# Kernel tuning notes

Measured on AMD Instinct MI355X. Metric: run time of the kernel, lower is better.

The kernel has to match this reference:

```python
import jax, jax.numpy as jnp
import numpy as np

N_GROUPS = 32
N_HEADS = 8
GN_EPS = 1e-5


def setup_inputs() -> dict:
    key = jax.random.key(0)
    k1, k2, k3 = jax.random.split(key, 3)
    B, C, H, W = 8, 512, 32, 32
    x = jax.random.normal(k1, (B, C, H, W), dtype=jnp.float32)
    gn_w = jnp.ones((C,), dtype=jnp.float32)
    gn_b = jnp.zeros((C,), dtype=jnp.float32)
    qkv_w = jax.random.normal(k2, (3 * C, C), dtype=jnp.float32) * 0.02
    qkv_b = jnp.zeros((3 * C,), dtype=jnp.float32)
    proj_w = jax.random.normal(k3, (C, C), dtype=jnp.float32) * 0.02
    proj_b = jnp.zeros((C,), dtype=jnp.float32)
    return {"x": x, "gn_w": gn_w, "gn_b": gn_b, "qkv_w": qkv_w,
            "qkv_b": qkv_b, "proj_w": proj_w, "proj_b": proj_b}


def reference(x, gn_w, gn_b, qkv_w, qkv_b, proj_w, proj_b):
    b, c, h, w = x.shape
    t = h * w
    xf = x.reshape(b, c, t)

    # GroupNorm(32, C) over (channel-group, spatial) dims
    xg = xf.reshape(b, N_GROUPS, (c // N_GROUPS) * t)
    mean = jnp.mean(xg, axis=-1, keepdims=True)
    var = jnp.var(xg, axis=-1, keepdims=True)
    normed = ((xg - mean) * jax.lax.rsqrt(var + GN_EPS)).reshape(b, c, t)
    normed = normed * gn_w[None, :, None] + gn_b[None, :, None]

    # 1x1 Conv1d -> matmul over channel dim
    qkv = jnp.einsum('oc,bct->bot', qkv_w, normed) + qkv_b[None, :, None]
    q, k, v = jnp.split(qkv, 3, axis=1)  # each [b, c, t]

    ch = c // N_HEADS
    scale = 1.0 / np.sqrt(np.sqrt(ch)).astype(np.float32)
    q = (q * scale).reshape(b * N_HEADS, ch, t)
    k = (k * scale).reshape(b * N_HEADS, ch, t)
    v = v.reshape(b * N_HEADS, ch, t)

    weight = jnp.einsum('bct,bcs->bts', q, k)
    weight = jax.nn.softmax(weight.astype(jnp.float32), axis=-1).astype(q.dtype)
    a = jnp.einsum('bts,bcs->bct', weight, v).reshape(b, c, t)

    # residual + 1x1 Conv2d projection
    out = jnp.einsum('oc,bct->bot', proj_w, xf + a) + proj_b[None, :, None]
    return out.reshape(b, -1, h, w)
```

## Files before the change

kernel.cpp:

```cpp
#include <hip/hip_runtime.h>

constexpr int B = 8;
constexpr int C = 512;
constexpr int T = 1024;
constexpr int CPG = 16;
constexpr int NH = 8;
constexpr int CH = 64;
constexpr float GN_EPS = 1e-5f;
constexpr float QSCALE = 0.18033688011112042f;

typedef __attribute__((ext_vector_type(4))) float f32x4;
typedef __attribute__((ext_vector_type(8))) short bf16x8;
typedef __attribute__((ext_vector_type(4))) short bf16x4;

__device__ inline short f2bf(float f) {
  union { float f; unsigned u; } v; v.f = f;
  unsigned r = (v.u + 0x7FFFu + ((v.u >> 16) & 1u)) >> 16;
  return (short)r;
}

__device__ inline unsigned cvt_pk_bf16(float a, float b) {
  unsigned r;
  asm("v_cvt_pk_bf16_f32 %0, %1, %2" : "=v"(r) : "v"(a), "v"(b));
  return r;
}

#define GLOAD16(gsrc, ldst) __builtin_amdgcn_global_load_lds( \
    (const __attribute__((address_space(1))) unsigned int*)(gsrc), \
    (__attribute__((address_space(3))) unsigned int*)(ldst), 16, 0, 0)

__global__ __launch_bounds__(256)
void gnw_kernel(const float* __restrict__ x, const float* __restrict__ gw,
                const float* __restrict__ gb, short* __restrict__ out,
                const float* __restrict__ qw, const float* __restrict__ pw,
                short* __restrict__ qwb, short* __restrict__ pwb) {
  const int bid = blockIdx.x;
  if (bid >= 256) {
    const int idx = (bid - 256) * 256 + threadIdx.x;
    constexpr int QW4 = 3 * C * C / 4;
    float4 v;
    short* dst;
    if (idx < QW4) {
      v = ((const float4*)qw)[idx];
      dst = qwb + (size_t)idx * 4;
    } else {
      v = ((const float4*)pw)[idx - QW4];
      dst = pwb + (size_t)(idx - QW4) * 4;
    }
    bf16x4 o;
    o[0] = f2bf(v.x); o[1] = f2bf(v.y); o[2] = f2bf(v.z); o[3] = f2bf(v.w);
    *(bf16x4*)dst = o;
    return;
  }
  const int b = bid >> 5;
  const int g = bid & 31;
  const float* xp = x + (size_t)(b * C + g * CPG) * T;
  const float4* x4 = (const float4*)xp;
  float s = 0.f, ss = 0.f;
  for (int i = threadIdx.x; i < CPG * T / 4; i += 256) {
    float4 v = x4[i];
    s  += v.x + v.y + v.z + v.w;
    ss += v.x * v.x + v.y * v.y + v.z * v.z + v.w * v.w;
  }
  #pragma unroll
  for (int o = 32; o; o >>= 1) {
    s  += __shfl_down(s, o);
    ss += __shfl_down(ss, o);
  }
  __shared__ float rs[4], rss[4];
  __shared__ float sm, sr;
  const int wid = threadIdx.x >> 6;
  if ((threadIdx.x & 63) == 0) { rs[wid] = s; rss[wid] = ss; }
  __syncthreads();
  if (threadIdx.x == 0) {
    float ts  = rs[0] + rs[1] + rs[2] + rs[3];
    float tss = rss[0] + rss[1] + rss[2] + rss[3];
    constexpr float inv_n = 1.f / (CPG * T);
    float mean = ts * inv_n;
    float var = tss * inv_n - mean * mean;
    sm = mean;
    sr = rsqrtf(var + GN_EPS);
  }
  __syncthreads();
  const float mean = sm, rstd = sr;

  const int tid = threadIdx.x;
  const int cl = tid >> 4;
  const int t4 = (tid & 15) * 4;
  const float cw = gw[g * CPG + cl] * rstd;
  const float cb = gb[g * CPG + cl] - mean * cw;
  __shared__ short tile[64][20];
  const int tr = tid >> 2;
  const int cq = (tid & 3) * 4;
  for (int t0 = 0; t0 < T; t0 += 64) {
    float4 v = x4[(cl * T + t0 + t4) >> 2];
    tile[t4 + 0][cl] = f2bf(v.x * cw + cb);
    tile[t4 + 1][cl] = f2bf(v.y * cw + cb);
    tile[t4 + 2][cl] = f2bf(v.z * cw + cb);
    tile[t4 + 3][cl] = f2bf(v.w * cw + cb);
    __syncthreads();
    *(bf16x4*)&out[((size_t)(b * T + t0 + tr)) * C + g * CPG + cq] =
        *(const bf16x4*)&tile[tr][cq];
    __syncthreads();
  }
}

__global__ __launch_bounds__(256)
void qkv_gemm(const short* __restrict__ Wb, const float* __restrict__ bias,
              const short* __restrict__ Xn, short* __restrict__ qb,
              short* __restrict__ kb, short* __restrict__ vb) {
  const int bid = blockIdx.x;
  const int b = bid & 7;
  const int rem = bid >> 3;
  const int o0 = (rem % 12) * 128;
  const int t0 = (rem / 12) * 128;
  const bool swap = (o0 >= 2 * C);
  __shared__ short Asm[128 * 64];
  __shared__ short Bsm[128 * 64];
  const int tid = threadIdx.x;
  const int wv = tid >> 6, lane = tid & 63;
  const int l15 = lane & 15, l4 = lane >> 4;
  const int wr = (wv >> 1) * 64, wc = (wv & 1) * 64;

  const short* gA[4]; const short* gB[4];
  char* lA[4]; char* lB[4];
  #pragma unroll
  for (int p = 0; p < 4; ++p) {
    const int off = p * 256 + tid;
    const int row = off >> 3;
    const int col = (off & 7) ^ (row & 7);
    gA[p] = Wb + (size_t)(o0 + row) * C + col * 8;
    gB[p] = Xn + ((size_t)b * T + t0 + row) * C + col * 8;
    lA[p] = (char*)Asm + (size_t)(p * 256 + (tid & ~63)) * 16;
    lB[p] = (char*)Bsm + (size_t)(p * 256 + (tid & ~63)) * 16;
  }

  f32x4 acc[4][4];
  #pragma unroll
  for (int i = 0; i < 4; ++i)
    #pragma unroll
    for (int j = 0; j < 4; ++j) acc[i][j] = f32x4{0.f, 0.f, 0.f, 0.f};

  for (int k0 = 0; k0 < C; k0 += 64) {
    #pragma unroll
    for (int p = 0; p < 4; ++p) {
      GLOAD16(gA[p] + k0, lA[p]);
      GLOAD16(gB[p] + k0, lB[p]);
    }
    __syncthreads();
    #pragma unroll
    for (int kk = 0; kk < 2; ++kk) {
      bf16x8 af[4], bfr[4];
      #pragma unroll
      for (int i = 0; i < 4; ++i) {
        const int sw = ((kk << 2) | l4) ^ (l15 & 7);
        af[i]  = *(const bf16x8*)&Asm[(wr + i * 16 + l15) * 64 + sw * 8];
        bfr[i] = *(const bf16x8*)&Bsm[(wc + i * 16 + l15) * 64 + sw * 8];
      }
      if (!swap) {
        #pragma unroll
        for (int fi = 0; fi < 4; ++fi)
          #pragma unroll
          for (int nj = 0; nj < 4; ++nj)
            acc[fi][nj] = __builtin_amdgcn_mfma_f32_16x16x32_bf16(
                af[fi], bfr[nj], acc[fi][nj], 0, 0, 0);
      } else {
        #pragma unroll
        for (int nj = 0; nj < 4; ++nj)
          #pragma unroll
          for (int fi = 0; fi < 4; ++fi)
            acc[nj][fi] = __builtin_amdgcn_mfma_f32_16x16x32_bf16(
                bfr[nj], af[fi], acc[nj][fi], 0, 0, 0);
      }
    }
    __syncthreads();
  }

  if (!swap) {
    short* dst = (o0 < C) ? qb : kb;
    const float sc = (o0 < C) ? QSCALE : 1.0f;
    #pragma unroll
    for (int fi = 0; fi < 4; ++fi) {
      const int ob = o0 + wr + fi * 16 + l4 * 4;
      const int bh = b * NH + ((ob >> 6) & 7);
      const int cb_ = ob & 63;
      #pragma unroll
      for (int nj = 0; nj < 4; ++nj) {
        const int tg = t0 + wc + nj * 16 + l15;
        bf16x4 pk;
        #pragma unroll
        for (int r = 0; r < 4; ++r)
          pk[r] = f2bf((acc[fi][nj][r] + bias[ob + r]) * sc);
        *(bf16x4*)&dst[((size_t)bh * T + tg) * CH + cb_] = pk;
      }
    }
  } else {
    #pragma unroll
    for (int fi = 0; fi < 4; ++fi) {
      const int ob = o0 + wr + fi * 16 + l15;
      const int bh = b * NH + ((ob >> 6) & 7);
      const int cb_ = ob & 63;
      const float bo = bias[ob];
      #pragma unroll
      for (int nj = 0; nj < 4; ++nj) {
        const int tg = t0 + wc + nj * 16 + l4 * 4;
        bf16x4 pk;
        #pragma unroll
        for (int r = 0; r < 4; ++r)
          pk[r] = f2bf(acc[nj][fi][r] + bo);
        *(bf16x4*)&vb[((size_t)bh * CH + cb_) * T + tg] = pk;
      }
    }
  }
}

__global__ __launch_bounds__(256)
void attn_kernel(const short* __restrict__ qb, const short* __restrict__ kb,
                 const short* __restrict__ vb, const float* __restrict__ x,
                 short* __restrict__ res) {
  const int bh = blockIdx.x & 63;
  const int tile = blockIdx.x >> 6;
  const int b = bh >> 3, h = bh & 7;
  const int t0 = tile * 128;
  const int tid = threadIdx.x;
  const int wv = tid >> 6;
  const int lane = tid & 63;
  const int l15 = lane & 15;
  const int l4 = lane >> 4;

  const short* qh = qb + (size_t)bh * T * CH;
  const short* kh = kb + (size_t)bh * T * CH;
  const short* vh = vb + (size_t)bh * CH * T;

  __shared__ short kt[2][64][64];
  __shared__ short vt[2][64][64];
  __shared__ short pl[4][2][16][64];
  short* plw = &pl[wv][0][0][0];

  const int sl_row[2] = { (0 * 256 + tid) >> 3, (1 * 256 + tid) >> 3 };
  const int sl_blk[2] = { (tid & 7) ^ (sl_row[0] & 7), (tid & 7) ^ (sl_row[1] & 7) };
  const int sl_lds[2] = { (0 * 256 + (tid & ~63)) * 8, (1 * 256 + (tid & ~63)) * 8 };

  bf16x8 qf[2][2];
  #pragma unroll
  for (int nj = 0; nj < 2; ++nj)
    #pragma unroll
    for (int ks = 0; ks < 2; ++ks)
      qf[nj][ks] = *(const bf16x8*)
          &qh[(size_t)(t0 + wv * 32 + nj * 16 + l15) * CH + ks * 32 + l4 * 8];

  f32x4 acc_o[2][4];
  #pragma unroll
  for (int nj = 0; nj < 2; ++nj)
    #pragma unroll
    for (int ct = 0; ct < 4; ++ct) acc_o[nj][ct] = f32x4{0.f, 0.f, 0.f, 0.f};
  float lsum[2] = {0.f, 0.f};

  #pragma unroll
  for (int p = 0; p < 2; ++p) {
    GLOAD16(kh + (size_t)sl_row[p] * CH + sl_blk[p] * 8, (char*)&kt[0][0][0] + sl_lds[p] * 2);
    GLOAD16(vh + (size_t)sl_row[p] * T + sl_blk[p] * 8, (char*)&vt[0][0][0] + sl_lds[p] * 2);
  }

  for (int it = 0; it < 16; ++it) {
    const int cur = it & 1;
    __syncthreads();
    if (it < 15) {
      const int s1 = (it + 1) * 64;
      #pragma unroll
      for (int p = 0; p < 2; ++p) {
        GLOAD16(kh + (size_t)(s1 + sl_row[p]) * CH + sl_blk[p] * 8,
                (char*)&kt[cur ^ 1][0][0] + sl_lds[p] * 2);
        GLOAD16(vh + (size_t)sl_row[p] * T + s1 + sl_blk[p] * 8,
                (char*)&vt[cur ^ 1][0][0] + sl_lds[p] * 2);
      }
    }
    const short* ktc = &kt[cur][0][0];
    const short* vtc = &vt[cur][0][0];

    f32x4 accs[2][4];
    #pragma unroll
    for (int nj = 0; nj < 2; ++nj)
      #pragma unroll
      for (int nt = 0; nt < 4; ++nt) accs[nj][nt] = f32x4{0.f, 0.f, 0.f, 0.f};
    __builtin_amdgcn_s_setprio(1);
    #pragma unroll
    for (int ks = 0; ks < 2; ++ks) {
      #pragma unroll
      for (int nt = 0; nt < 4; ++nt) {
        bf16x8 kf = *(const bf16x8*)
            &ktc[(nt * 16 + l15) * 64 + (((ks << 2) | l4) ^ (l15 & 7)) * 8];
        accs[0][nt] = __builtin_amdgcn_mfma_f32_16x16x32_bf16(kf, qf[0][ks], accs[0][nt], 0, 0, 0);
        accs[1][nt] = __builtin_amdgcn_mfma_f32_16x16x32_bf16(kf, qf[1][ks], accs[1][nt], 0, 0, 0);
      }
    }
    __builtin_amdgcn_s_setprio(0);

    f32x4 p4[2][4];
    #pragma unroll
    for (int nj = 0; nj < 2; ++nj) {
      #pragma unroll
      for (int nt = 0; nt < 4; ++nt)
        #pragma unroll
        for (int r = 0; r < 4; ++r)
          p4[nj][nt][r] = __builtin_amdgcn_exp2f(accs[nj][nt][r]);
      f32x4 sv;
      #pragma unroll
      for (int r = 0; r < 4; ++r)
        sv[r] = (p4[nj][0][r] + p4[nj][1][r]) + (p4[nj][2][r] + p4[nj][3][r]);
      lsum[nj] += (sv[0] + sv[1]) + (sv[2] + sv[3]);
      #pragma unroll
      for (int nt = 0; nt < 4; ++nt) {
        uint2 w;
        w.x = cvt_pk_bf16(p4[nj][nt][0], p4[nj][nt][1]);
        w.y = cvt_pk_bf16(p4[nj][nt][2], p4[nj][nt][3]);
        *(uint2*)&plw[nj * 1024 + l15 * 64 +
                      ((nt * 2 + (l4 >> 1)) ^ (l15 & 7)) * 8 + (l4 & 1) * 4] = w;
      }
    }

    __builtin_amdgcn_s_setprio(1);
    #pragma unroll
    for (int ks = 0; ks < 2; ++ks) {
      const int psl = (((ks << 2) | l4) ^ (l15 & 7)) * 8;
      bf16x8 pf0 = *(const bf16x8*)&plw[l15 * 64 + psl];
      bf16x8 pf1 = *(const bf16x8*)&plw[1024 + l15 * 64 + psl];
      #pragma unroll
      for (int ct = 0; ct < 4; ++ct) {
        bf16x8 vf = *(const bf16x8*)
            &vtc[(ct * 16 + l15) * 64 + (((ks << 2) | l4) ^ (l15 & 7)) * 8];
        acc_o[0][ct] = __builtin_amdgcn_mfma_f32_16x16x32_bf16(vf, pf0, acc_o[0][ct], 0, 0, 0);
        acc_o[1][ct] = __builtin_amdgcn_mfma_f32_16x16x32_bf16(vf, pf1, acc_o[1][ct], 0, 0, 0);
      }
    }
    __builtin_amdgcn_s_setprio(0);
  }

  #pragma unroll
  for (int nj = 0; nj < 2; ++nj) {
    float l = lsum[nj];
    l += __shfl_xor(l, 16);
    l += __shfl_xor(l, 32);
    const float inv = 1.f / l;
    const int trow = t0 + wv * 32 + nj * 16 + l15;
    #pragma unroll
    for (int ct = 0; ct < 4; ++ct) {
      const int cbase = h * CH + ct * 16 + l4 * 4;
      bf16x4 pk;
      #pragma unroll
      for (int r = 0; r < 4; ++r) {
        const float xv = x[((size_t)(b * C + cbase + r)) * T + trow];
        pk[r] = f2bf(acc_o[nj][ct][r] * inv + xv);
      }
      *(bf16x4*)&res[((size_t)(b * T + trow)) * C + cbase] = pk;
    }
  }
}

__global__ __launch_bounds__(256)
void proj_gemm(const short* __restrict__ Wp, const float* __restrict__ bias,
               const short* __restrict__ Rs, float* __restrict__ out) {
  const int bid = blockIdx.x;
  const int b = bid & 7;
  const int rem = bid >> 3;
  const int o0 = (rem & 3) * 128;
  const int t0 = (rem >> 2) * 64;
  __shared__ short Asm[128 * 64];
  __shared__ short Bsm[64 * 64];
  const int tid = threadIdx.x;
  const int wv = tid >> 6, lane = tid & 63;
  const int l15 = lane & 15, l4 = lane >> 4;
  const int wr = (wv >> 1) * 64;
  const int wc = (wv & 1) * 32;

  const short* gA[4]; const short* gB[2];
  char* lA[4]; char* lB[2];
  #pragma unroll
  for (int p = 0; p < 4; ++p) {
    const int off = p * 256 + tid;
    const int row = off >> 3;
    const int col = (off & 7) ^ (row & 7);
    gA[p] = Wp + (size_t)(o0 + row) * C + col * 8;
    lA[p] = (char*)Asm + (size_t)(p * 256 + (tid & ~63)) * 16;
  }
  #pragma unroll
  for (int p = 0; p < 2; ++p) {
    const int off = p * 256 + tid;
    const int row = off >> 3;
    const int col = (off & 7) ^ (row & 7);
    gB[p] = Rs + ((size_t)b * T + t0 + row) * C + col * 8;
    lB[p] = (char*)Bsm + (size_t)(p * 256 + (tid & ~63)) * 16;
  }

  f32x4 acc[2][4];
  #pragma unroll
  for (int i = 0; i < 2; ++i)
    #pragma unroll
    for (int j = 0; j < 4; ++j) acc[i][j] = f32x4{0.f, 0.f, 0.f, 0.f};

  for (int k0 = 0; k0 < C; k0 += 64) {
    #pragma unroll
    for (int p = 0; p < 4; ++p) GLOAD16(gA[p] + k0, lA[p]);
    #pragma unroll
    for (int p = 0; p < 2; ++p) GLOAD16(gB[p] + k0, lB[p]);
    __syncthreads();
    #pragma unroll
    for (int kk = 0; kk < 2; ++kk) {
      const int sw = ((kk << 2) | l4) ^ (l15 & 7);
      bf16x8 af[4], bfr[2];
      #pragma unroll
      for (int i = 0; i < 4; ++i)
        af[i] = *(const bf16x8*)&Asm[(wr + i * 16 + l15) * 64 + sw * 8];
      #pragma unroll
      for (int j = 0; j < 2; ++j)
        bfr[j] = *(const bf16x8*)&Bsm[(wc + j * 16 + l15) * 64 + sw * 8];
      __builtin_amdgcn_s_setprio(1);
      #pragma unroll
      for (int nj = 0; nj < 2; ++nj)
        #pragma unroll
        for (int fi = 0; fi < 4; ++fi)
          acc[nj][fi] = __builtin_amdgcn_mfma_f32_16x16x32_bf16(
              bfr[nj], af[fi], acc[nj][fi], 0, 0, 0);
      __builtin_amdgcn_s_setprio(0);
    }
    __syncthreads();
  }

  #pragma unroll
  for (int fi = 0; fi < 4; ++fi) {
    const int o = o0 + wr + fi * 16 + l15;
    const float bo = bias[o];
    #pragma unroll
    for (int nj = 0; nj < 2; ++nj) {
      const int tg = t0 + wc + nj * 16 + l4 * 4;
      f32x4 vo;
      #pragma unroll
      for (int r = 0; r < 4; ++r) vo[r] = acc[nj][fi][r] + bo;
      *(f32x4*)&out[((size_t)(b * C + o)) * T + tg] = vo;
    }
  }
}

extern "C" void kernel_launch(void* const* d_in, const int* in_sizes, int n_in,
                              void* d_out, int out_size, void* d_ws, size_t ws_size,
                              hipStream_t stream) {
  const float* x      = (const float*)d_in[0];
  const float* gn_w   = (const float*)d_in[1];
  const float* gn_b   = (const float*)d_in[2];
  const float* qkv_w  = (const float*)d_in[3];
  const float* qkv_b  = (const float*)d_in[4];
  const float* proj_w = (const float*)d_in[5];
  const float* proj_b = (const float*)d_in[6];
  float* out = (float*)d_out;

  constexpr size_t MB = 1 << 20;
  char* w = (char*)d_ws;
  short* normed = (short*)w;
  short* qbuf   = (short*)(w + 8 * MB);
  short* kbuf   = (short*)(w + 16 * MB);
  short* vbuf   = (short*)(w + 24 * MB);
  short* resb   = (short*)(w + 32 * MB);
  short* qwb    = (short*)(w + 40 * MB);
  short* pwb    = (short*)(w + 40 * MB + (size_t)3 * C * C * 2);

  gnw_kernel<<<dim3(1280), 256, 0, stream>>>(x, gn_w, gn_b, normed,
                                             qkv_w, proj_w, qwb, pwb);
  qkv_gemm<<<dim3(768), 256, 0, stream>>>(qwb, qkv_b, normed, qbuf, kbuf, vbuf);
  attn_kernel<<<dim3(B * NH * (T / 128)), 256, 0, stream>>>(qbuf, kbuf, vbuf, x, resb);
  proj_gemm<<<dim3(512), 256, 0, stream>>>(pwb, proj_b, resb, out);
}
```

Before: 85.03 us.

## Halve QKV GEMM tile width and stage two KV tiles per attention sync

The QKV GEMM now uses 128x64 tiles and launches twice as many blocks (1536). This gives more parallelism across CUs, and MFMA phases are wrapped in setprio. The attention kernel moves to dynamic shared memory (80KB) with four K/V buffers. It processes two 64-key tiles per barrier and prefetches the next pair, halving syncs at the cost of more LDS per block and lower occupancy.

Result: slower. 93.87 us (+10.4%).

```diff
diff --git a/kernel.cpp b/kernel.cpp
--- a/kernel.cpp
+++ b/kernel.cpp
@@ -113,65 +113,72 @@
   const int b = bid & 7;
   const int rem = bid >> 3;
   const int o0 = (rem % 12) * 128;
-  const int t0 = (rem / 12) * 128;
+  const int t0 = (rem / 12) * 64;
   const bool swap = (o0 >= 2 * C);
   __shared__ short Asm[128 * 64];
-  __shared__ short Bsm[128 * 64];
+  __shared__ short Bsm[64 * 64];
   const int tid = threadIdx.x;
   const int wv = tid >> 6, lane = tid & 63;
   const int l15 = lane & 15, l4 = lane >> 4;
-  const int wr = (wv >> 1) * 64, wc = (wv & 1) * 64;
-
-  const short* gA[4]; const short* gB[4];
-  char* lA[4]; char* lB[4];
+  const int wr = (wv >> 1) * 64;
+  const int wc = (wv & 1) * 32;
+
+  const short* gA[4]; const short* gB[2];
+  char* lA[4]; char* lB[2];
   #pragma unroll
   for (int p = 0; p < 4; ++p) {
     const int off = p * 256 + tid;
     const int row = off >> 3;
     const int col = (off & 7) ^ (row & 7);
     gA[p] = Wb + (size_t)(o0 + row) * C + col * 8;
+    lA[p] = (char*)Asm + (size_t)(p * 256 + (tid & ~63)) * 16;
+  }
+  #pragma unroll
+  for (int p = 0; p < 2; ++p) {
+    const int off = p * 256 + tid;
+    const int row = off >> 3;
+    const int col = (off & 7) ^ (row & 7);
     gB[p] = Xn + ((size_t)b * T + t0 + row) * C + col * 8;
-    lA[p] = (char*)Asm + (size_t)(p * 256 + (tid & ~63)) * 16;
     lB[p] = (char*)Bsm + (size_t)(p * 256 + (tid & ~63)) * 16;
   }
 
-  f32x4 acc[4][4];
-  #pragma unroll
-  for (int i = 0; i < 4; ++i)
-    #pragma unroll
-    for (int j = 0; j < 4; ++j) acc[i][j] = f32x4{0.f, 0.f, 0.f, 0.f};
+  f32x4 acc[8];
+  #pragma unroll
+  for (int i = 0; i < 8; ++i) acc[i] = f32x4{0.f, 0.f, 0.f, 0.f};
 
   for (int k0 = 0; k0 < C; k0 += 64) {
     #pragma unroll
-    for (int p = 0; p < 4; ++p) {
-      GLOAD16(gA[p] + k0, lA[p]);
-      GLOAD16(gB[p] + k0, lB[p]);
-    }
+    for (int p = 0; p < 4; ++p) GLOAD16(gA[p] + k0, lA[p]);
+    #pragma unroll
+    for (int p = 0; p < 2; ++p) GLOAD16(gB[p] + k0, lB[p]);
     __syncthreads();
     #pragma unroll
     for (int kk = 0; kk < 2; ++kk) {
-      bf16x8 af[4], bfr[4];
-      #pragma unroll
-      for (int i = 0; i < 4; ++i) {
-        const int sw = ((kk << 2) | l4) ^ (l15 & 7);
-        af[i]  = *(const bf16x8*)&Asm[(wr + i * 16 + l15) * 64 + sw * 8];
-        bfr[i] = *(const bf16x8*)&Bsm[(wc + i * 16 + l15) * 64 + sw * 8];
-      }
+      const int sw = ((kk << 2) | l4) ^ (l15 & 7);
+      bf16x8 af[4], bfr[2];
+      #pragma unroll
+      for (int i = 0; i < 4; ++i)
+        af[i] = *(const bf16x8*)&Asm[(wr + i * 16 + l15) * 64 + sw * 8];
+      #pragma unroll
+      for (int j = 0; j < 2; ++j)
+        bfr[j] = *(const bf16x8*)&Bsm[(wc + j * 16 + l15) * 64 + sw * 8];
+      __builtin_amdgcn_s_setprio(1);
       if (!swap) {
         #pragma unroll
         for (int fi = 0; fi < 4; ++fi)
           #pragma unroll
-          for (int nj = 0; nj < 4; ++nj)
-            acc[fi][nj] = __builtin_amdgcn_mfma_f32_16x16x32_bf16(
-                af[fi], bfr[nj], acc[fi][nj], 0, 0, 0);
+          for (int nj = 0; nj < 2; ++nj)
+            acc[fi * 2 + nj] = __builtin_amdgcn_mfma_f32_16x16x32_bf16(
+                af[fi], bfr[nj], acc[fi * 2 + nj], 0, 0, 0);
       } else {
         #pragma unroll
-        for (int nj = 0; nj < 4; ++nj)
+        for (int nj = 0; nj < 2; ++nj)
           #pragma unroll
           for (int fi = 0; fi < 4; ++fi)
-            acc[nj][fi] = __builtin_amdgcn_mfma_f32_16x16x32_bf16(
-                bfr[nj], af[fi], acc[nj][fi], 0, 0, 0);
-      }
+            acc[nj * 4 + fi] = __builtin_amdgcn_mfma_f32_16x16x32_bf16(
+                bfr[nj], af[fi], acc[nj * 4 + fi], 0, 0, 0);
+      }
+      __builtin_amdgcn_s_setprio(0);
     }
     __syncthreads();
   }
@@ -185,12 +192,12 @@
       const int bh = b * NH + ((ob >> 6) & 7);
       const int cb_ = ob & 63;
       #pragma unroll
-      for (int nj = 0; nj < 4; ++nj) {
+      for (int nj = 0; nj < 2; ++nj) {
         const int tg = t0 + wc + nj * 16 + l15;
         bf16x4 pk;
         #pragma unroll
         for (int r = 0; r < 4; ++r)
-          pk[r] = f2bf((acc[fi][nj][r] + bias[ob + r]) * sc);
+          pk[r] = f2bf((acc[fi * 2 + nj][r] + bias[ob + r]) * sc);
         *(bf16x4*)&dst[((size_t)bh * T + tg) * CH + cb_] = pk;
       }
     }
@@ -202,12 +209,12 @@
       const int cb_ = ob & 63;
       const float bo = bias[ob];
       #pragma unroll
-      for (int nj = 0; nj < 4; ++nj) {
+      for (int nj = 0; nj < 2; ++nj) {
         const int tg = t0 + wc + nj * 16 + l4 * 4;
         bf16x4 pk;
         #pragma unroll
         for (int r = 0; r < 4; ++r)
-          pk[r] = f2bf(acc[nj][fi][r] + bo);
+          pk[r] = f2bf(acc[nj * 4 + fi][r] + bo);
         *(bf16x4*)&vb[((size_t)bh * CH + cb_) * T + tg] = pk;
       }
     }
@@ -232,14 +239,14 @@
   const short* kh = kb + (size_t)bh * T * CH;
   const short* vh = vb + (size_t)bh * CH * T;
 
-  __shared__ short kt[2][64][64];
-  __shared__ short vt[2][64][64];
-  __shared__ short pl[4][2][16][64];
-  short* plw = &pl[wv][0][0][0];
+  extern __shared__ short smem[];
+  short* ktb = smem;
+  short* vtb = smem + 4 * 4096;
+  short* plw = smem + 8 * 4096 + wv * 2048;
 
   const int sl_row[2] = { (0 * 256 + tid) >> 3, (1 * 256 + tid) >> 3 };
   const int sl_blk[2] = { (tid & 7) ^ (sl_row[0] & 7), (tid & 7) ^ (sl_row[1] & 7) };
-  const int sl_lds[2] = { (0 * 256 + (tid & ~63)) * 8, (1 * 256 + (tid & ~63)) * 8 };
+  const int sl_lds[2] = { (0 * 256 + (tid & ~63)) * 16, (1 * 256 + (tid & ~63)) * 16 };
 
   bf16x8 qf[2][2];
   #pragma unroll
@@ -257,83 +264,96 @@
   float lsum[2] = {0.f, 0.f};
 
   #pragma unroll
-  for (int p = 0; p < 2; ++p) {
-    GLOAD16(kh + (size_t)sl_row[p] * CH + sl_blk[p] * 8, (char*)&kt[0][0][0] + sl_lds[p] * 2);
-    GLOAD16(vh + (size_t)sl_row[p] * T + sl_blk[p] * 8, (char*)&vt[0][0][0] + sl_lds[p] * 2);
-  }
-
-  for (int it = 0; it < 16; ++it) {
-    const int cur = it & 1;
-    __syncthreads();
-    if (it < 15) {
-      const int s1 = (it + 1) * 64;
-      #pragma unroll
-      for (int p = 0; p < 2; ++p) {
-        GLOAD16(kh + (size_t)(s1 + sl_row[p]) * CH + sl_blk[p] * 8,
-                (char*)&kt[cur ^ 1][0][0] + sl_lds[p] * 2);
-        GLOAD16(vh + (size_t)sl_row[p] * T + s1 + sl_blk[p] * 8,
-                (char*)&vt[cur ^ 1][0][0] + sl_lds[p] * 2);
-      }
-    }
-    const short* ktc = &kt[cur][0][0];
-    const short* vtc = &vt[cur][0][0];
-
-    f32x4 accs[2][4];
-    #pragma unroll
-    for (int nj = 0; nj < 2; ++nj)
-      #pragma unroll
-      for (int nt = 0; nt < 4; ++nt) accs[nj][nt] = f32x4{0.f, 0.f, 0.f, 0.f};
-    __builtin_amdgcn_s_setprio(1);
-    #pragma unroll
-    for (int ks = 0; ks < 2; ++ks) {
-      #pragma unroll
-      for (int nt = 0; nt < 4; ++nt) {
-        bf16x8 kf = *(const bf16x8*)
-            &ktc[(nt * 16 + l15) * 64 + (((ks << 2) | l4) ^ (l15 & 7)) * 8];
-        accs[0][nt] = __builtin_amdgcn_mfma_f32_16x16x32_bf16(kf, qf[0][ks], accs[0][nt], 0, 0, 0);
-        accs[1][nt] = __builtin_amdgcn_mfma_f32_16x16x32_bf16(kf, qf[1][ks], accs[1][nt], 0, 0, 0);
-      }
-    }
-    __builtin_amdgcn_s_setprio(0);
-
-    f32x4 p4[2][4];
-    #pragma unroll
-    for (int nj = 0; nj < 2; ++nj) {
-      #pragma unroll
-      for (int nt = 0; nt < 4; ++nt)
+  for (int j = 0; j < 2; ++j) {
+    #pragma unroll
+    for (int p = 0; p < 2; ++p) {
+      GLOAD16(kh + (size_t)(j * 64 + sl_row[p]) * CH + sl_blk[p] * 8,
+              (char*)(ktb + j * 4096) + sl_lds[p]);
+      GLOAD16(vh + (size_t)sl_row[p] * T + j * 64 + sl_blk[p] * 8,
+              (char*)(vtb + j * 4096) + sl_lds[p]);
+    }
+  }
+
+  for (int g = 0; g < 8; ++g) {
+    const int pr = (g & 1) * 2;
+    __syncthreads();
+    if (g < 7) {
+      const int tt = 2 * g + 2;
+      #pragma unroll
+      for (int j = 0; j < 2; ++j) {
+        const int bf = (pr ^ 2) + j;
+        #pragma unroll
+        for (int p = 0; p < 2; ++p) {
+          GLOAD16(kh + (size_t)((tt + j) * 64 + sl_row[p]) * CH + sl_blk[p] * 8,
+                  (char*)(ktb + bf * 4096) + sl_lds[p]);
+          GLOAD16(vh + (size_t)sl_row[p] * T + (tt + j) * 64 + sl_blk[p] * 8,
+                  (char*)(vtb + bf * 4096) + sl_lds[p]);
+        }
+      }
+    }
+
+    #pragma unroll
+    for (int j = 0; j < 2; ++j) {
+      const short* ktc = ktb + (pr + j) * 4096;
+      const short* vtc = vtb + (pr + j) * 4096;
+
+      f32x4 accs[2][4];
+      #pragma unroll
+      for (int nj = 0; nj < 2; ++nj)
+        #pragma unroll
+        for (int nt = 0; nt < 4; ++nt) accs[nj][nt] = f32x4{0.f, 0.f, 0.f, 0.f};
+      __builtin_amdgcn_s_setprio(1);
+      #pragma unroll
+      for (int ks = 0; ks < 2; ++ks) {
+        #pragma unroll
+        for (int nt = 0; nt < 4; ++nt) {
+          bf16x8 kf = *(const bf16x8*)
+              &ktc[(nt * 16 + l15) * 64 + (((ks << 2) | l4) ^ (l15 & 7)) * 8];
+          accs[0][nt] = __builtin_amdgcn_mfma_f32_16x16x32_bf16(kf, qf[0][ks], accs[0][nt], 0, 0, 0);
+          accs[1][nt] = __builtin_amdgcn_mfma_f32_16x16x32_bf16(kf, qf[1][ks], accs[1][nt], 0, 0, 0);
+        }
+      }
+      __builtin_amdgcn_s_setprio(0);
+
+      f32x4 p4[2][4];
+      #pragma unroll
+      for (int nj = 0; nj < 2; ++nj) {
+        #pragma unroll
+        for (int nt = 0; nt < 4; ++nt)
+          #pragma unroll
+          for (int r = 0; r < 4; ++r)
+            p4[nj][nt][r] = __builtin_amdgcn_exp2f(accs[nj][nt][r]);
+        f32x4 sv;
         #pragma unroll
         for (int r = 0; r < 4; ++r)
-          p4[nj][nt][r] = __builtin_amdgcn_exp2f(accs[nj][nt][r]);
-      f32x4 sv;
-      #pragma unroll
-      for (int r = 0; r < 4; ++r)
-        sv[r] = (p4[nj][0][r] + p4[nj][1][r]) + (p4[nj][2][r] + p4[nj][3][r]);
-      lsum[nj] += (sv[0] + sv[1]) + (sv[2] + sv[3]);
-      #pragma unroll
-      for (int nt = 0; nt < 4; ++nt) {
-        uint2 w;
-        w.x = cvt_pk_bf16(p4[nj][nt][0], p4[nj][nt][1]);
-        w.y = cvt_pk_bf16(p4[nj][nt][2], p4[nj][nt][3]);
-        *(uint2*)&plw[nj * 1024 + l15 * 64 +
-                      ((nt * 2 + (l4 >> 1)) ^ (l15 & 7)) * 8 + (l4 & 1) * 4] = w;
-      }
-    }
-
-    __builtin_amdgcn_s_setprio(1);
-    #pragma unroll
-    for (int ks = 0; ks < 2; ++ks) {
-      const int psl = (((ks << 2) | l4) ^ (l15 & 7)) * 8;
-      bf16x8 pf0 = *(const bf16x8*)&plw[l15 * 64 + psl];
-      bf16x8 pf1 = *(const bf16x8*)&plw[1024 + l15 * 64 + psl];
-      #pragma unroll
-      for (int ct = 0; ct < 4; ++ct) {
-        bf16x8 vf = *(const bf16x8*)
-            &vtc[(ct * 16 + l15) * 64 + (((ks << 2) | l4) ^ (l15 & 7)) * 8];
-        acc_o[0][ct] = __builtin_amdgcn_mfma_f32_16x16x32_bf16(vf, pf0, acc_o[0][ct], 0, 0, 0);
-        acc_o[1][ct] = __builtin_amdgcn_mfma_f32_16x16x32_bf16(vf, pf1, acc_o[1][ct], 0, 0, 0);
-      }
-    }
-    __builtin_amdgcn_s_setprio(0);
+          sv[r] = (p4[nj][0][r] + p4[nj][1][r]) + (p4[nj][2][r] + p4[nj][3][r]);
+        lsum[nj] += (sv[0] + sv[1]) + (sv[2] + sv[3]);
+        #pragma unroll
+        for (int nt = 0; nt < 4; ++nt) {
+          uint2 w;
+          w.x = cvt_pk_bf16(p4[nj][nt][0], p4[nj][nt][1]);
+          w.y = cvt_pk_bf16(p4[nj][nt][2], p4[nj][nt][3]);
+          *(uint2*)&plw[nj * 1024 + l15 * 64 +
+                        ((nt * 2 + (l4 >> 1)) ^ (l15 & 7)) * 8 + (l4 & 1) * 4] = w;
+        }
+      }
+
+      __builtin_amdgcn_s_setprio(1);
+      #pragma unroll
+      for (int ks = 0; ks < 2; ++ks) {
+        const int psl = (((ks << 2) | l4) ^ (l15 & 7)) * 8;
+        bf16x8 pf0 = *(const bf16x8*)&plw[l15 * 64 + psl];
+        bf16x8 pf1 = *(const bf16x8*)&plw[1024 + l15 * 64 + psl];
+        #pragma unroll
+        for (int ct = 0; ct < 4; ++ct) {
+          bf16x8 vf = *(const bf16x8*)
+              &vtc[(ct * 16 + l15) * 64 + (((ks << 2) | l4) ^ (l15 & 7)) * 8];
+          acc_o[0][ct] = __builtin_amdgcn_mfma_f32_16x16x32_bf16(vf, pf0, acc_o[0][ct], 0, 0, 0);
+          acc_o[1][ct] = __builtin_amdgcn_mfma_f32_16x16x32_bf16(vf, pf1, acc_o[1][ct], 0, 0, 0);
+        }
+      }
+      __builtin_amdgcn_s_setprio(0);
+    }
   }
 
   #pragma unroll
@@ -465,7 +485,7 @@
 
   gnw_kernel<<<dim3(1280), 256, 0, stream>>>(x, gn_w, gn_b, normed,
                                              qkv_w, proj_w, qwb, pwb);
-  qkv_gemm<<<dim3(768), 256, 0, stream>>>(qwb, qkv_b, normed, qbuf, kbuf, vbuf);
-  attn_kernel<<<dim3(B * NH * (T / 128)), 256, 0, stream>>>(qbuf, kbuf, vbuf, x, resb);
+  qkv_gemm<<<dim3(1536), 256, 0, stream>>>(qwb, qkv_b, normed, qbuf, kbuf, vbuf);
+  attn_kernel<<<dim3(B * NH * (T / 128)), 256, 81920, stream>>>(qbuf, kbuf, vbuf, x, resb);
   proj_gemm<<<dim3(512), 256, 0, stream>>>(pwb, proj_b, resb, out);
 }
```
